# Kernel optimization log

Measured on AMD Instinct MI355X. Metric: run time of the kernel, lower is better.

The kernel has to match this reference:

```python
import jax, jax.numpy as jnp
import numpy as np

B, L, CM, CZ, NC = 1, 512, 256, 128, 128
N_BINS = 65  # rel-pos bins for offsets in [-32, 32]


def setup_inputs() -> dict:
    key = jax.random.key(0)
    ks = jax.random.split(key, 11)
    s = 0.02
    return {
        "target_feat": jax.random.normal(ks[0], (B, 20, L), jnp.float32),
        "residue_index": jnp.arange(L, dtype=jnp.int32)[None, :],  # [B, L]
        "msa_feat": jax.random.normal(ks[1], (B, 21, L), jnp.float32),
        "w_a_w": jax.random.normal(ks[2], (CZ, 20), jnp.float32) * s,
        "w_a_b": jax.random.normal(ks[3], (CZ,), jnp.float32) * s,
        "w_b_w": jax.random.normal(ks[4], (CZ, 20), jnp.float32) * s,
        "w_b_b": jax.random.normal(ks[5], (CZ,), jnp.float32) * s,
        "w_p_w": jax.random.normal(ks[6], (CZ, N_BINS), jnp.float32) * s,
        "w_p_b": jax.random.normal(ks[7], (CZ,), jnp.float32) * s,
        "w_clust_w": jax.random.normal(ks[8], (NC, CM, 21), jnp.float32) * s,
        "w_clust_b": jax.random.normal(ks[9], (NC, CM), jnp.float32) * s,
        "w_m_w": jax.random.normal(ks[10], (CM, 20), jnp.float32) * s,
        "w_m_b": jnp.zeros((CM,), jnp.float32),
    }


def reference(target_feat, residue_index, msa_feat,
              w_a_w, w_a_b, w_b_w, w_b_b,
              w_p_w, w_p_b, w_clust_w, w_clust_b,
              w_m_w, w_m_b):
    # 1x1 Conv1d == per-position linear over channels
    a = jnp.einsum('cf,bfl->bcl', w_a_w, target_feat) + w_a_b[None, :, None]  # [B,CZ,L]
    b = jnp.einsum('cf,bfl->bcl', w_b_w, target_feat) + w_b_b[None, :, None]
    # outer sum pair representation: a_i + b_j  -> [B,CZ,L,L]
    pair_rep = a[:, :, :, None] + b[:, :, None, :]
    # relative position: argmin(|d - v_bins|) over bins == clip(d,-32,32)+32;
    # one-hot @ 1x1-conv weight == embedding gather of w_p columns
    d = residue_index[:, :, None] - residue_index[:, None, :]  # [B,L,L]
    bins = jnp.clip(d, -32, 32) + 32
    p = jnp.take(w_p_w.T, bins, axis=0)  # [B,L,L,CZ]
    pair_rep = pair_rep + jnp.transpose(p, (0, 3, 1, 2)) + w_p_b[None, :, None, None]
    # per-cluster 1x1 convs on the SAME msa_feat -> one batched GEMM
    # w_clust_w: [NC,CM,21], msa_feat: [B,21,L] -> [B,CM,NC,L]
    msa_rep = jnp.einsum('kcf,bfl->bckl', w_clust_w, msa_feat) \
        + w_clust_b.T[None, :, :, None]
    msa_rep = msa_rep + (jnp.einsum('cf,bfl->bcl', w_m_w, target_feat)
                         + w_m_b[None, :, None])[:, :, None, :]
    return (msa_rep, pair_rep)
```

## Files before the change

kernel.cpp:

```cpp
#include <hip/hip_runtime.h>

#define L 512
#define CM 256
#define CZ 128
#define NC 128
#define NBINS 65

typedef float  f4 __attribute__((ext_vector_type(4)));
typedef float  f2 __attribute__((ext_vector_type(2)));
typedef int    i4 __attribute__((ext_vector_type(4)));


__global__ void pre_kernel(const float* __restrict__ tf,
                           const float* __restrict__ waw,
                           const float* __restrict__ wab,
                           const float* __restrict__ wbw,
                           const float* __restrict__ wbb,
                           const float* __restrict__ wpb,
                           const float* __restrict__ wmw,
                           const float* __restrict__ wmb,
                           float* __restrict__ a2,
                           float* __restrict__ b2,
                           float* __restrict__ m2) {
    int idx = blockIdx.x * 256 + threadIdx.x;
    if (idx < CZ * L) {
        int c = idx >> 9, l = idx & (L - 1);
        float acc = wab[c] + wpb[c];
        #pragma unroll
        for (int f = 0; f < 20; ++f)
            acc += waw[c * 20 + f] * tf[f * L + l];
        a2[idx] = acc;
    } else if (idx < 2 * CZ * L) {
        int t = idx - CZ * L;
        int c = t >> 9, l = t & (L - 1);
        float acc = wbb[c];
        #pragma unroll
        for (int f = 0; f < 20; ++f)
            acc += wbw[c * 20 + f] * tf[f * L + l];
        b2[t] = acc;
    } else {
        int t = idx - 2 * CZ * L;
        int c = t >> 9, l = t & (L - 1);
        float acc = wmb[c];
        #pragma unroll
        for (int f = 0; f < 20; ++f)
            acc += wmw[c * 20 + f] * tf[f * L + l];
        m2[t] = acc;
    }
}

#define PAIR_BLKS 2048
#define MSA_BLKS  2048

__global__ __launch_bounds__(256)
void fused_kernel(const float* __restrict__ a2,
                  const float* __restrict__ b2,
                  const float* __restrict__ wpw,
                  const int* __restrict__ ri,
                  const float* __restrict__ mf,
                  const float* __restrict__ wc,
                  const float* __restrict__ wcb,
                  const float* __restrict__ m2,
                  float* __restrict__ pair_out,
                  float* __restrict__ msa_out) {
    int bx = blockIdx.x;
    int t = threadIdx.x;

    if (bx < PAIR_BLKS) {
        int c  = bx >> 4;
        int i0 = (bx & 15) * 32;

        __shared__ float swp[NBINS];
        __shared__ float sa[32];
        __shared__ int   sri[32];

        if (t < NBINS)             swp[t]       = wpw[c * NBINS + t];
        if (t >= 128 && t < 160)   sa[t - 128]  = a2[c * L + i0 + (t - 128)];
        if (t >= 192 && t < 224)   sri[t - 192] = ri[i0 + (t - 192)];

        int half = t >> 7;
        int j0   = (t & 127) * 4;

        i4 rj = *reinterpret_cast<const i4*>(&ri[j0]);
        f4 bb = *reinterpret_cast<const f4*>(&b2[c * L + j0]);

        __syncthreads();

        size_t base0 = ((size_t)c * L + (i0 + half)) * L + j0;

        #pragma unroll
        for (int r = 0; r < 16; ++r) {
            int il = r * 2 + half;
            float ai  = sa[il];
            int   rii = sri[il];

            int d0 = min(max(rii - rj.x, -32), 32) + 32;
            int d1 = min(max(rii - rj.y, -32), 32) + 32;
            int d2 = min(max(rii - rj.z, -32), 32) + 32;
            int d3 = min(max(rii - rj.w, -32), 32) + 32;

            f4 o;
            o.x = ai + bb.x + swp[d0];
            o.y = ai + bb.y + swp[d1];
            o.z = ai + bb.z + swp[d2];
            o.w = ai + bb.w + swp[d3];

            __builtin_nontemporal_store(
                o, reinterpret_cast<f4*>(&pair_out[base0 + (size_t)r * (2 * L)]));
        }
    } else {
        int b  = bx - PAIR_BLKS;
        int c  = b >> 3;
        int k0 = (b & 7) * 16;
        int l0 = t * 2;

        float mfa[21], mfb[21];
        #pragma unroll
        for (int f = 0; f < 21; ++f) {
            f2 u = *reinterpret_cast<const f2*>(&mf[f * L + l0]);
            mfa[f] = u.x;
            mfb[f] = u.y;
        }
        f2 mm = *reinterpret_cast<const f2*>(&m2[c * L + l0]);

        #pragma unroll 4
        for (int kk = 0; kk < 16; ++kk) {
            int k = k0 + kk;
            const float* w = &wc[((size_t)k * CM + c) * 21];
            float bias = wcb[k * CM + c];
            float acc0 = bias + mm.x;
            float acc1 = bias + mm.y;
            #pragma unroll
            for (int f = 0; f < 21; ++f) {
                float wf = w[f];
                acc0 += wf * mfa[f];
                acc1 += wf * mfb[f];
            }
            f2 o;
            o.x = acc0;
            o.y = acc1;
            __builtin_nontemporal_store(
                o, reinterpret_cast<f2*>(&msa_out[((size_t)(c * NC + k)) * L + l0]));
        }
    }
}

extern "C" void kernel_launch(void* const* d_in, const int* in_sizes, int n_in,
                              void* d_out, int out_size, void* d_ws, size_t ws_size,
                              hipStream_t stream) {
    const float* tf  = (const float*)d_in[0];
    const int*   ri  = (const int*)d_in[1];
    const float* mf  = (const float*)d_in[2];
    const float* waw = (const float*)d_in[3];
    const float* wab = (const float*)d_in[4];
    const float* wbw = (const float*)d_in[5];
    const float* wbb = (const float*)d_in[6];
    const float* wpw = (const float*)d_in[7];
    const float* wpb = (const float*)d_in[8];
    const float* wc  = (const float*)d_in[9];
    const float* wcb = (const float*)d_in[10];
    const float* wmw = (const float*)d_in[11];
    const float* wmb = (const float*)d_in[12];

    float* out = (float*)d_out;
    float* msa_out  = out;
    float* pair_out = out + (size_t)CM * NC * L;

    float* a2 = (float*)d_ws;
    float* b2 = a2 + CZ * L;
    float* m2 = b2 + CZ * L;

    pre_kernel<<<dim3((2 * CZ * L + CM * L) / 256), dim3(256), 0, stream>>>(
        tf, waw, wab, wbw, wbb, wpb, wmw, wmb, a2, b2, m2);

    fused_kernel<<<dim3(PAIR_BLKS + MSA_BLKS), dim3(256), 0, stream>>>(
        a2, b2, wpw, ri, mf, wc, wcb, m2, pair_out, msa_out);
}
```

Before: 243.4 us.

## Fuse pre-projection into main kernel and interleave pair/msa blocks

```diff
diff --git a/kernel.cpp b/kernel.cpp
--- a/kernel.cpp
+++ b/kernel.cpp
@@ -11,78 +11,65 @@
 typedef int    i4 __attribute__((ext_vector_type(4)));
 
 
-__global__ void pre_kernel(const float* __restrict__ tf,
-                           const float* __restrict__ waw,
-                           const float* __restrict__ wab,
-                           const float* __restrict__ wbw,
-                           const float* __restrict__ wbb,
-                           const float* __restrict__ wpb,
-                           const float* __restrict__ wmw,
-                           const float* __restrict__ wmb,
-                           float* __restrict__ a2,
-                           float* __restrict__ b2,
-                           float* __restrict__ m2) {
-    int idx = blockIdx.x * 256 + threadIdx.x;
-    if (idx < CZ * L) {
-        int c = idx >> 9, l = idx & (L - 1);
-        float acc = wab[c] + wpb[c];
-        #pragma unroll
-        for (int f = 0; f < 20; ++f)
-            acc += waw[c * 20 + f] * tf[f * L + l];
-        a2[idx] = acc;
-    } else if (idx < 2 * CZ * L) {
-        int t = idx - CZ * L;
-        int c = t >> 9, l = t & (L - 1);
-        float acc = wbb[c];
-        #pragma unroll
-        for (int f = 0; f < 20; ++f)
-            acc += wbw[c * 20 + f] * tf[f * L + l];
-        b2[t] = acc;
-    } else {
-        int t = idx - 2 * CZ * L;
-        int c = t >> 9, l = t & (L - 1);
-        float acc = wmb[c];
-        #pragma unroll
-        for (int f = 0; f < 20; ++f)
-            acc += wmw[c * 20 + f] * tf[f * L + l];
-        m2[t] = acc;
-    }
-}
+__global__ __launch_bounds__(256)
+void fused_all(const float* __restrict__ tf,
+               const int*   __restrict__ ri,
+               const float* __restrict__ mf,
+               const float* __restrict__ waw,
+               const float* __restrict__ wab,
+               const float* __restrict__ wbw,
+               const float* __restrict__ wbb,
+               const float* __restrict__ wpw,
+               const float* __restrict__ wpb,
+               const float* __restrict__ wc,
+               const float* __restrict__ wcb,
+               const float* __restrict__ wmw,
+               const float* __restrict__ wmb,
+               float* __restrict__ pair_out,
+               float* __restrict__ msa_out) {
+    int bx = blockIdx.x;
+    int t  = threadIdx.x;
 
-#define PAIR_BLKS 2048
-#define MSA_BLKS  2048
-
-__global__ __launch_bounds__(256)
-void fused_kernel(const float* __restrict__ a2,
-                  const float* __restrict__ b2,
-                  const float* __restrict__ wpw,
-                  const int* __restrict__ ri,
-                  const float* __restrict__ mf,
-                  const float* __restrict__ wc,
-                  const float* __restrict__ wcb,
-                  const float* __restrict__ m2,
-                  float* __restrict__ pair_out,
-                  float* __restrict__ msa_out) {
-    int bx = blockIdx.x;
-    int t = threadIdx.x;
-
-    if (bx < PAIR_BLKS) {
-        int c  = bx >> 4;
-        int i0 = (bx & 15) * 32;
+    if ((bx & 1) == 0) {
+        int p  = bx >> 1;
+        int c  = p >> 4;
+        int i0 = (p & 15) * 32;
 
         __shared__ float swp[NBINS];
         __shared__ float sa[32];
         __shared__ int   sri[32];
 
-        if (t < NBINS)             swp[t]       = wpw[c * NBINS + t];
-        if (t >= 128 && t < 160)   sa[t - 128]  = a2[c * L + i0 + (t - 128)];
-        if (t >= 192 && t < 224)   sri[t - 192] = ri[i0 + (t - 192)];
+        if (t < NBINS) swp[t] = wpw[c * NBINS + t];
+        if (t >= 128 && t < 160) {
+            int i = i0 + (t - 128);
+            float acc = wab[c] + wpb[c];
+            const float* wa = &waw[c * 20];
+            #pragma unroll
+            for (int f = 0; f < 20; ++f)
+                acc += wa[f] * tf[f * L + i];
+            sa[t - 128] = acc;
+        }
+        if (t >= 192 && t < 224) sri[t - 192] = ri[i0 + (t - 192)];
 
         int half = t >> 7;
         int j0   = (t & 127) * 4;
 
+        f4 bb;
+        {
+            float b0 = wbb[c];
+            bb.x = b0; bb.y = b0; bb.z = b0; bb.w = b0;
+            const float* wb = &wbw[c * 20];
+            #pragma unroll
+            for (int f = 0; f < 20; ++f) {
+                f4 tv = *reinterpret_cast<const f4*>(&tf[f * L + j0]);
+                float w = wb[f];
+                bb.x += w * tv.x;
+                bb.y += w * tv.y;
+                bb.z += w * tv.z;
+                bb.w += w * tv.w;
+            }
+        }
         i4 rj = *reinterpret_cast<const i4*>(&ri[j0]);
-        f4 bb = *reinterpret_cast<const f4*>(&b2[c * L + j0]);
 
         __syncthreads();
 
@@ -109,9 +96,9 @@
                 o, reinterpret_cast<f4*>(&pair_out[base0 + (size_t)r * (2 * L)]));
         }
     } else {
-        int b  = bx - PAIR_BLKS;
-        int c  = b >> 3;
-        int k0 = (b & 7) * 16;
+        int m  = bx >> 1;
+        int c  = m >> 3;
+        int k0 = (m & 7) * 16;
         int l0 = t * 2;
 
         float mfa[21], mfb[21];
@@ -121,7 +108,19 @@
             mfa[f] = u.x;
             mfb[f] = u.y;
         }
-        f2 mm = *reinterpret_cast<const f2*>(&m2[c * L + l0]);
+        f2 mm;
+        {
+            float m0 = wmb[c];
+            mm.x = m0; mm.y = m0;
+            const float* wm = &wmw[c * 20];
+            #pragma unroll
+            for (int f = 0; f < 20; ++f) {
+                f2 u = *reinterpret_cast<const f2*>(&tf[f * L + l0]);
+                float w = wm[f];
+                mm.x += w * u.x;
+                mm.y += w * u.y;
+            }
+        }
 
         #pragma unroll 4
         for (int kk = 0; kk < 16; ++kk) {
@@ -166,13 +165,7 @@
     float* msa_out  = out;
     float* pair_out = out + (size_t)CM * NC * L;
 
-    float* a2 = (float*)d_ws;
-    float* b2 = a2 + CZ * L;
-    float* m2 = b2 + CZ * L;
-
-    pre_kernel<<<dim3((2 * CZ * L + CM * L) / 256), dim3(256), 0, stream>>>(
-        tf, waw, wab, wbw, wbb, wpb, wmw, wmb, a2, b2, m2);
-
-    fused_kernel<<<dim3(PAIR_BLKS + MSA_BLKS), dim3(256), 0, stream>>>(
-        a2, b2, wpw, ri, mf, wc, wcb, m2, pair_out, msa_out);
+    fused_all<<<dim3(4096), dim3(256), 0, stream>>>(
+        tf, ri, mf, waw, wab, wbw, wbb, wpw, wpb, wc, wcb, wmw, wmb,
+        pair_out, msa_out);
 }
```

New measurement: 246.9 us. Within noise of the previous version (+1.4%).
